# Performance work log

Hardware: AMD Instinct MI355X
Metric: run time of the kernel (lower is better)

## Reference

```python
import jax, jax.numpy as jnp
import numpy as np
import math

N_EMBD = 1024
N_HEAD = 16
B, T = 4, 2048

def setup_inputs() -> dict:
    key = jax.random.key(0)
    k1, k2, k3, k4, k5 = jax.random.split(key, 5)
    C = N_EMBD
    scale_in = 1.0 / math.sqrt(C)
    x = jax.random.normal(k1, (B, T, C), dtype=jnp.float32)
    W_attn = jax.random.normal(k2, (C, 3 * C), dtype=jnp.float32) * scale_in
    b_attn = jax.random.normal(k3, (3 * C,), dtype=jnp.float32) * 0.02
    W_proj = jax.random.normal(k4, (C, C), dtype=jnp.float32) * scale_in
    b_proj = jax.random.normal(k5, (C,), dtype=jnp.float32) * 0.02
    attention_mask = jnp.ones((B, T), dtype=jnp.int32)
    return {"x": x, "W_attn": W_attn, "b_attn": b_attn,
            "W_proj": W_proj, "b_proj": b_proj,
            "attention_mask": attention_mask}

def reference(x, W_attn, b_attn, W_proj, b_proj, attention_mask):
    Bx, Tx, C = x.shape
    H = N_HEAD
    D = C // H
    qkv = x @ W_attn + b_attn                      # [B,T,3C]
    q, k, v = jnp.split(qkv, 3, axis=-1)
    # [B,H,T,D]
    q = q.reshape(Bx, Tx, H, D).transpose(0, 2, 1, 3)
    k = k.reshape(Bx, Tx, H, D).transpose(0, 2, 1, 3)
    v = v.reshape(Bx, Tx, H, D).transpose(0, 2, 1, 3)
    att = jnp.einsum('bhqd,bhkd->bhqk', q, k) * (1.0 / math.sqrt(D))
    causal = jnp.tril(jnp.ones((Tx, Tx), dtype=bool))  # [T,T]
    neg_inf = jnp.float32(-jnp.inf)
    att = jnp.where(causal[None, None, :, :], att, neg_inf)
    pad = (attention_mask != 0)[:, None, None, :]      # [B,1,1,T]
    att = jnp.where(pad, att, neg_inf)
    att = jax.nn.softmax(att, axis=-1)
    y = jnp.einsum('bhqk,bhkd->bhqd', att, v)          # [B,H,T,D]
    y = y.transpose(0, 2, 1, 3).reshape(Bx, Tx, C)
    y = y @ W_proj + b_proj
    return y
```

## Files before the change

### kernel.cpp

```cpp
#include <hip/hip_runtime.h>
#include <hip/hip_bf16.h>
#include <stdint.h>

#define B_ 4
#define T_ 2048
#define C_ 1024
#define H_ 16
#define D_ 64
#define BH_ (B_*H_)
#define M_ (B_*T_)

typedef __attribute__((ext_vector_type(8))) short short8;
typedef __attribute__((ext_vector_type(4))) float f32x4;
typedef __attribute__((ext_vector_type(16))) float f32x16;

#if __has_builtin(__builtin_amdgcn_exp2f)
#define EXP2(x) __builtin_amdgcn_exp2f(x)
#else
#define EXP2(x) exp2f(x)
#endif

#define QSCALE 0.18033688011112043f

__device__ __forceinline__ unsigned short f2bf(float f) {
  union { float f; unsigned int u; } v; v.f = f;
  unsigned int r = v.u + 0x7FFFu + ((v.u >> 16) & 1u);
  return (unsigned short)(r >> 16);
}

__device__ __forceinline__ unsigned int cvtpk_bf16(float lo, float hi) {
  unsigned int r;
  asm("v_cvt_pk_bf16_f32 %0, %1, %2" : "=v"(r) : "v"(lo), "v"(hi));
  return r;
}

__device__ __forceinline__ void gload_lds16(const void* g, void* l) {
  __builtin_amdgcn_global_load_lds(
      (__attribute__((address_space(1))) void*)g,
      (__attribute__((address_space(3))) void*)l, 16, 0, 0);
}

__global__ __launch_bounds__(256) void k_cvt(const float* __restrict__ in,
                                             unsigned short* __restrict__ out, int n) {
  int i = (blockIdx.x * 256 + threadIdx.x) * 4;
  if (i >= n) return;
  float4 v = *reinterpret_cast<const float4*>(in + i);
  union { unsigned short u[4]; unsigned long long ll; } o;
  o.u[0] = f2bf(v.x); o.u[1] = f2bf(v.y); o.u[2] = f2bf(v.z); o.u[3] = f2bf(v.w);
  *reinterpret_cast<unsigned long long*>(out + i) = o.ll;
}

__global__ __launch_bounds__(256) void k_tr(const float* __restrict__ W,
                                            unsigned short* __restrict__ Wt, int K, int N) {
  __shared__ float t[32][33];
  int n0 = blockIdx.x * 32, k0 = blockIdx.y * 32;
  int tx = threadIdx.x, ty = threadIdx.y;
  #pragma unroll
  for (int j = 0; j < 4; j++)
    t[ty + j*8][tx] = W[(size_t)(k0 + ty + j*8) * N + n0 + tx];
  __syncthreads();
  #pragma unroll
  for (int j = 0; j < 4; j++)
    Wt[(size_t)(n0 + ty + j*8) * K + k0 + tx] = f2bf(t[tx][ty + j*8]);
}

template<int QKV>
__global__ __launch_bounds__(512) void k_gemm8(const unsigned short* __restrict__ A,
                                               const unsigned short* __restrict__ Bt,
                                               const float* __restrict__ bias,
                                               void* __restrict__ outp, int N, int K) {
  __shared__ __align__(16) unsigned short Al[2][128*64];
  __shared__ __align__(16) unsigned short Bl[2][256*64];

  const int tid = threadIdx.x;
  const int lane = tid & 63, wv = tid >> 6;
  const int lg = lane >> 4, lr = lane & 15;
  const int wm = wv >> 2, wn = wv & 3;

  const int nwg = gridDim.x * gridDim.y;
  const int l = blockIdx.y * gridDim.x + blockIdx.x;
  const int wg = (l & 7) * (nwg >> 3) + (l >> 3);
  const int m0 = (wg / gridDim.x) * 128;
  const int n0 = (wg % gridDim.x) * 256;

  const int NT = K >> 6;

  auto stageA = [&](int s, int t, int h) {
    int row = tid >> 3, g = tid & 7;
    int gsw = g ^ (row & 7);
    gload_lds16(A + (size_t)(m0 + h*64 + row) * K + t*64 + gsw*8,
                (char*)Al[s] + h*8192 + tid*16);
  };
  auto stageB = [&](int s, int t, int h) {
    #pragma unroll
    for (int u = 0; u < 2; ++u) {
      int gi = tid + u*512;
      int row = gi >> 3, g = gi & 7;
      int gsw = g ^ (row & 7);
      gload_lds16(Bt + (size_t)(n0 + h*128 + row) * K + t*64 + gsw*8,
                  (char*)Bl[s] + h*16384 + gi*16);
    }
  };

  f32x4 acc[2][2][2][2];
  #pragma unroll
  for (int i = 0; i < 2; ++i)
    #pragma unroll
    for (int j = 0; j < 2; ++j)
      #pragma unroll
      for (int p = 0; p < 2; ++p)
        #pragma unroll
        for (int q = 0; q < 2; ++q) acc[i][j][p][q] = (f32x4){0.f,0.f,0.f,0.f};

  stageA(0, 0, 0); stageB(0, 0, 0); stageA(0, 0, 1); stageB(0, 0, 1);
  if (NT > 1) { stageB(1, 1, 0); stageA(1, 1, 0); }
  asm volatile("s_waitcnt vmcnt(3)" ::: "memory");
  __builtin_amdgcn_s_barrier();

#define GPH(MhC, NhC, STAGE, ISPH4, VMOK)  do {                                 \
    short8 af_[2][2], bf_[2][2];                                                \
    _Pragma("unroll") for (int mf = 0; mf < 2; ++mf) {                          \
      int rA = (MhC)*64 + wm*32 + mf*16 + lr;                                   \
      int r7 = rA & 7;                                                          \
      af_[mf][0] = *(const short8*)(Asb + rA*128 + ((lg      ^ r7) << 4));      \
      af_[mf][1] = *(const short8*)(Asb + rA*128 + (((4|lg) ^ r7) << 4));       \
    }                                                                           \
    _Pragma("unroll") for (int nf = 0; nf < 2; ++nf) {                          \
      int rB = (NhC)*128 + wn*32 + nf*16 + lr;                                  \
      int r7 = rB & 7;                                                          \
      bf_[nf][0] = *(const short8*)(Bsb + rB*128 + ((lg      ^ r7) << 4));      \
      bf_[nf][1] = *(const short8*)(Bsb + rB*128 + (((4|lg) ^ r7) << 4));       \
    }                                                                           \
    STAGE;                                                                      \
    __builtin_amdgcn_s_barrier();                                               \
    asm volatile("s_waitcnt lgkmcnt(0)" ::: "memory");                          \
    __builtin_amdgcn_sched_barrier(0);                                          \
    __builtin_amdgcn_s_setprio(1);                                              \
    _Pragma("unroll") for (int mf = 0; mf < 2; ++mf)                            \
      _Pragma("unroll") for (int nf = 0; nf < 2; ++nf) {                        \
        acc[MhC][NhC][mf][nf] = __builtin_amdgcn_mfma_f32_16x16x32_bf16(        \
            af_[mf][0], bf_[nf][0], acc[MhC][NhC][mf][nf], 0, 0, 0);            \
        acc[MhC][NhC][mf][nf] = __builtin_amdgcn_mfma_f32_16x16x32_bf16(        \
            af_[mf][1], bf_[nf][1], acc[MhC][NhC][mf][nf], 0, 0, 0);            \
      }                                                                         \
    __builtin_amdgcn_s_setprio(0);                                              \
    if (ISPH4) {                                                                \
      if (VMOK) asm volatile("s_waitcnt vmcnt(3)" ::: "memory");                \
      else      asm volatile("s_waitcnt vmcnt(0)" ::: "memory");                \
    }                                                                           \
    __builtin_amdgcn_s_barrier();                                               \
  } while (0)

  for (int t = 0; t < NT; ++t) {
    const char* Asb = (const char*)Al[t & 1];
    const char* Bsb = (const char*)Bl[t & 1];
    const int s0 = t & 1, s1 = s0 ^ 1;
    const bool p1 = (t + 1 < NT), p2 = (t + 2 < NT);
    GPH(0, 0, if (p1) stageA(s1, t+1, 1), 0, 0);
    GPH(1, 0, if (p1) stageB(s1, t+1, 1), 0, 0);
    GPH(0, 1, if (p2) stageB(s0, t+2, 0), 0, 0);
    GPH(1, 1, if (p2) stageA(s0, t+2, 0), 1, p2);
  }
#undef GPH

  if (QKV) {
    unsigned short* qb = (unsigned short*)outp;
    const size_t SZ = (size_t)BH_ * T_ * D_;
    #pragma unroll
    for (int Mh = 0; Mh < 2; ++Mh)
      #pragma unroll
      for (int mf = 0; mf < 2; ++mf) {
        int mb = m0 + Mh*64 + wm*32 + mf*16 + lg*4;
        #pragma unroll
        for (int Nh = 0; Nh < 2; ++Nh)
          #pragma unroll
          for (int nf = 0; nf < 2; ++nf) {
            int n = n0 + Nh*128 + wn*32 + nf*16 + lr;
            float bv = bias[n];
            int which = n >> 10, c = n & 1023, h = c >> 6, d = c & 63;
            unsigned short* base = qb + (size_t)which * SZ;
            #pragma unroll
            for (int r = 0; r < 4; ++r) {
              int m = mb + r;
              int bb2 = m >> 11, tt = m & 2047;
              float y = acc[Mh][Nh][mf][nf][r] + bv;
              if (which == 0) y *= QSCALE;
              base[((size_t)(bb2*H_ + h)*T_ + tt)*D_ + d] = f2bf(y);
            }
          }
      }
  } else {
    float* out = (float*)outp;
    #pragma unroll
    for (int Mh = 0; Mh < 2; ++Mh)
      #pragma unroll
      for (int mf = 0; mf < 2; ++mf) {
        int mb = m0 + Mh*64 + wm*32 + mf*16 + lg*4;
        #pragma unroll
        for (int Nh = 0; Nh < 2; ++Nh)
          #pragma unroll
          for (int nf = 0; nf < 2; ++nf) {
            int n = n0 + Nh*128 + wn*32 + nf*16 + lr;
            float bv = bias[n];
            #pragma unroll
            for (int r = 0; r < 4; ++r)
              out[(size_t)(mb + r)*N + n] = acc[Mh][Nh][mf][nf][r] + bv;
          }
      }
  }
}

__global__ __launch_bounds__(256, 2) void k_attn4(const unsigned short* __restrict__ Qb,
                                                  const unsigned short* __restrict__ Kb,
                                                  const unsigned short* __restrict__ Vb,
                                                  const int* __restrict__ amask,
                                                  unsigned short* __restrict__ Yb) {
  __shared__ __align__(16) char pool[32768];

  const int l = blockIdx.y * 16 + blockIdx.x;
  const int local = l >> 3;
  const int tq = 15 - (local >> 3);
  const int bh = (l & 7) * 8 + (local & 7);
  const int bb = bh >> 4, hh = bh & 15;

  const int tid = threadIdx.x;
  const int lane = tid & 63, w = tid >> 6;
  const int hi = lane >> 5, l31 = lane & 31;

  const unsigned short* Qh = Qb + (size_t)bh * (T_*D_);
  const unsigned short* Kh = Kb + (size_t)bh * (T_*D_);
  const unsigned short* Vh = Vb + (size_t)bh * (T_*D_);

  const int kvp = tid & 31, d0v = (tid >> 5) * 8;

  auto stage_load = [&](int i, int b, short8& sv0, short8& sv1, int& nm) {
    const int kv0 = i << 6;
    char* base = pool + b * 16384;
    #pragma unroll
    for (int s = 0; s < 2; ++s) {
      int gi = tid + s * 256;
      int row = gi >> 3, gc = gi & 7;
      gload_lds16(Kh + (size_t)(kv0 + row)*D_ + (gc ^ (row & 7)) * 8, base + gi * 16);
    }
    int kv = kv0 + 2 * kvp;
    sv0 = *reinterpret_cast<const short8*>(Vh + (size_t)kv*D_ + d0v);
    sv1 = *reinterpret_cast<const short8*>(Vh + (size_t)(kv + 1)*D_ + d0v);
    nm = amask[bb*T_ + kv0 + lane];
  };
  auto stage_write = [&](int b, short8 sv0, short8 sv1) {
    unsigned int* vt = (unsigned int*)(pool + b * 16384 + 8192);
    #pragma unroll
    for (int jj = 0; jj < 8; ++jj) {
      int d = d0v + jj;
      unsigned int wd = (unsigned short)sv0[jj] | ((unsigned int)(unsigned short)sv1[jj] << 16);
      vt[d * 32 + (kvp ^ ((d & 7) << 2))] = wd;
    }
  };

  const int nT = 2 * tq + 2;
  const int qbase = tq << 7;
  const int qw = qbase + w * 32;
  const int q  = qw + l31;

  short8 qf[4];
  #pragma unroll
  for (int dt = 0; dt < 4; ++dt)
    qf[dt] = *reinterpret_cast<const short8*>(Qh + (size_t)q*D_ + dt*16 + hi*8);

  f32x16 o0, o1;
  #pragma unroll
  for (int r = 0; r < 16; ++r) { o0[r] = 0.f; o1[r] = 0.f; }
  float mr = -1e30f, ls = 0.f;

  short8 sv0, sv1; int cm;
  stage_load(0, 0, sv0, sv1, cm);
  stage_write(0, sv0, sv1);
  __syncthreads();

  for (int i = 0; i < nT; ++i) {
    const int b = i & 1;
    const bool pf = (i + 1 < nT);
    short8 nv0, nv1; int nm = 0;
    if (pf) stage_load(i + 1, b ^ 1, nv0, nv1, nm);
    const int kv0 = i << 6;

    if (kv0 <= qw + 31) {
      const unsigned short* Klb = (const unsigned short*)(pool + b * 16384);
      const char* Vtb = pool + b * 16384 + 8192;

      f32x16 st0, st1;
      #pragma unroll
      for (int r = 0; r < 16; ++r) { st0[r] = 0.f; st1[r] = 0.f; }
      __builtin_amdgcn_s_setprio(1);
      #pragma unroll
      for (int dt = 0; dt < 4; ++dt) {
        int gg = dt * 2 + hi;
        int ra = l31;
        short8 kf0 = *reinterpret_cast<const short8*>(Klb + ra*64 + (gg ^ (ra & 7)) * 8);
        st0 = __builtin_amdgcn_mfma_f32_32x32x16_bf16(kf0, qf[dt], st0, 0, 0, 0);
        int rb = 32 + l31;
        short8 kf1 = *reinterpret_cast<const short8*>(Klb + rb*64 + (gg ^ (rb & 7)) * 8);
        st1 = __builtin_amdgcn_mfma_f32_32x32x16_bf16(kf1, qf[dt], st1, 0, 0, 0);
      }
      __builtin_amdgcn_s_setprio(0);

      if (kv0 + 63 > qw) {
        #pragma unroll
        for (int r = 0; r < 16; ++r) {
          int kvl = (r & 3) + 8 * (r >> 2) + 4 * hi;
          if (kv0 + kvl      > q) st0[r] = -1e30f;
          if (kv0 + 32 + kvl > q) st1[r] = -1e30f;
        }
      }
      unsigned long long mb = __ballot(cm != 0);
      if (mb != ~0ull) {
        #pragma unroll
        for (int r = 0; r < 16; ++r) {
          int kvl = (r & 3) + 8 * (r >> 2) + 4 * hi;
          if (!((mb >> kvl) & 1))        st0[r] = -1e30f;
          if (!((mb >> (kvl + 32)) & 1)) st1[r] = -1e30f;
        }
      }

      float mm[8];
      #pragma unroll
      for (int r = 0; r < 8; ++r)
        mm[r] = fmaxf(fmaxf(st0[r], st0[r + 8]), fmaxf(st1[r], st1[r + 8]));
      #pragma unroll
      for (int s = 4; s > 0; s >>= 1)
        #pragma unroll
        for (int r = 0; r < s; ++r) mm[r] = fmaxf(mm[r], mm[r + s]);
      float mo = fmaxf(mm[0], __shfl_xor(mm[0], 32));
      if (!__all(mo <= mr + 8.0f)) {
        float mnew = fmaxf(mr, mo);
        float corr = EXP2(mr - mnew);
        ls *= corr;
        #pragma unroll
        for (int r = 0; r < 16; ++r) { o0[r] *= corr; o1[r] *= corr; }
        mr = mnew;
      }
      float rs = 0.f;
      #pragma unroll
      for (int r = 0; r < 16; ++r) {
        st0[r] = EXP2(st0[r] - mr); rs += st0[r];
        st1[r] = EXP2(st1[r] - mr); rs += st1[r];
      }
      rs += __shfl_xor(rs, 32);
      ls += rs;

      unsigned int pw[2][4][2];
      #pragma unroll
      for (int a = 0; a < 4; ++a) {
        pw[0][a][0] = cvtpk_bf16(st0[4*a],   st0[4*a+1]);
        pw[0][a][1] = cvtpk_bf16(st0[4*a+2], st0[4*a+3]);
        pw[1][a][0] = cvtpk_bf16(st1[4*a],   st1[4*a+1]);
        pw[1][a][1] = cvtpk_bf16(st1[4*a+2], st1[4*a+3]);
      }

      #pragma unroll
      for (int kt = 0; kt < 4; ++kt) {
        const int t = kt >> 1, h2 = kt & 1;
        unsigned int send0 = hi ? pw[t][2*h2][0]   : pw[t][2*h2+1][0];
        unsigned int send1 = hi ? pw[t][2*h2][1]   : pw[t][2*h2+1][1];
        unsigned int own0  = hi ? pw[t][2*h2+1][0] : pw[t][2*h2][0];
        unsigned int own1  = hi ? pw[t][2*h2+1][1] : pw[t][2*h2][1];
        unsigned int recv0 = __shfl_xor(send0, 32);
        unsigned int recv1 = __shfl_xor(send1, 32);
        union { unsigned int u[4]; short8 v; } pf2;
        pf2.u[0] = hi ? recv0 : own0;
        pf2.u[1] = hi ? recv1 : own1;
        pf2.u[2] = hi ? own0  : recv0;
        pf2.u[3] = hi ? own1  : recv1;
        int gg = kt * 2 + hi;
        int dA = l31;
        short8 vf0 = *reinterpret_cast<const short8*>(Vtb + dA*128 + ((gg ^ (dA & 7)) * 16));
        int dB = 32 + l31;
        short8 vf1 = *reinterpret_cast<const short8*>(Vtb + dB*128 + ((gg ^ (dB & 7)) * 16));
        __builtin_amdgcn_s_setprio(1);
        o0 = __builtin_amdgcn_mfma_f32_32x32x16_bf16(vf0, pf2.v, o0, 0, 0, 0);
        o1 = __builtin_amdgcn_mfma_f32_32x32x16_bf16(vf1, pf2.v, o1, 0, 0, 0);
        __builtin_amdgcn_s_setprio(0);
      }
    }
    if (pf) { stage_write(b ^ 1, nv0, nv1); cm = nm; }
    __syncthreads();
  }

  float inv = 1.0f / ls;
  size_t rowbase = ((size_t)bb*T_ + q)*C_ + hh*D_;
  #pragma unroll
  for (int a = 0; a < 4; ++a) {
    union { unsigned short h[4]; unsigned long long ll; } y0, y1;
    #pragma unroll
    for (int bq = 0; bq < 4; ++bq) {
      int r = 4*a + bq;
      y0.h[bq] = f2bf(o0[r] * inv);
      y1.h[bq] = f2bf(o1[r] * inv);
    }
    int d0o = 8*a + 4*hi;
    *reinterpret_cast<unsigned long long*>(Yb + rowbase + d0o)      = y0.ll;
    *reinterpret_cast<unsigned long long*>(Yb + rowbase + 32 + d0o) = y1.ll;
  }
}

extern "C" void kernel_launch(void* const* d_in, const int* in_sizes, int n_in,
                              void* d_out, int out_size, void* d_ws, size_t ws_size,
                              hipStream_t stream) {
  const float* x      = (const float*)d_in[0];
  const float* W_attn = (const float*)d_in[1];
  const float* b_attn = (const float*)d_in[2];
  const float* W_proj = (const float*)d_in[3];
  const float* b_proj = (const float*)d_in[4];
  const int*   amask  = (const int*)d_in[5];
  float* out = (float*)d_out;

  char* ws = (char*)d_ws;
  size_t off = 0;
  auto alloc = [&](size_t bytes) { char* p = ws + off; off += (bytes + 255) & ~(size_t)255; return p; };
  unsigned short* xb   = (unsigned short*)alloc((size_t)M_ * C_ * 2);
  unsigned short* Wta  = (unsigned short*)alloc((size_t)3 * C_ * C_ * 2);
  unsigned short* Wtp  = (unsigned short*)alloc((size_t)C_ * C_ * 2);
  unsigned short* qkvb = (unsigned short*)alloc((size_t)3 * BH_ * T_ * D_ * 2);
  unsigned short* Yb   = (unsigned short*)alloc((size_t)M_ * C_ * 2);

  k_cvt<<<(M_ * C_) / 1024, 256, 0, stream>>>(x, xb, M_ * C_);
  k_tr<<<dim3(3*C_/32, C_/32), dim3(32, 8), 0, stream>>>(W_attn, Wta, C_, 3*C_);
  k_tr<<<dim3(C_/32,  C_/32),  dim3(32, 8), 0, stream>>>(W_proj, Wtp, C_, C_);

  k_gemm8<1><<<dim3(3*C_/256, M_/128), 512, 0, stream>>>(xb, Wta, b_attn, qkvb, 3*C_, C_);

  unsigned short* Qb = qkvb;
  unsigned short* Kb = qkvb + (size_t)BH_ * T_ * D_;
  unsigned short* Vb = qkvb + 2 * (size_t)BH_ * T_ * D_;
  k_attn4<<<dim3(16, BH_/1), 256, 0, stream>>>(Qb, Kb, Vb, amask, Yb);

  k_gemm8<0><<<dim3(C_/256, M_/128), 512, 0, stream>>>(Yb, Wtp, b_proj, out, C_, C_);
}
```

Before: 187.5 us.

## Reshape GEMM tile to 256x128 with per-wave 128x32 sub-tiles and B-fragment reuse

Both projection GEMMs now use a 256x128 output tile instead of 128x256. Each wave owns a 128x32 sub-tile, and its B fragments are loaded from LDS once per K-step and reused across two M-halves, which cuts LDS read traffic per MFMA. The pipeline drops from four phases with two-deep prefetch to two phases with one-step-ahead prefetch, and vmcnt waits are adjusted to match. This lowers LDS pressure and barrier count, but leaves less time to hide global-load latency, and the grid shape changes for both GEMMs.

```diff
diff --git a/kernel.cpp b/kernel.cpp
--- a/kernel.cpp
+++ b/kernel.cpp
@@ -69,8 +69,8 @@
                                                const unsigned short* __restrict__ Bt,
                                                const float* __restrict__ bias,
                                                void* __restrict__ outp, int N, int K) {
-  __shared__ __align__(16) unsigned short Al[2][128*64];
-  __shared__ __align__(16) unsigned short Bl[2][256*64];
+  __shared__ __align__(16) unsigned short Al[2][256*64];
+  __shared__ __align__(16) unsigned short Bl[2][128*64];
 
   const int tid = threadIdx.x;
   const int lane = tid & 63, wv = tid >> 6;
@@ -80,86 +80,78 @@
   const int nwg = gridDim.x * gridDim.y;
   const int l = blockIdx.y * gridDim.x + blockIdx.x;
   const int wg = (l & 7) * (nwg >> 3) + (l >> 3);
-  const int m0 = (wg / gridDim.x) * 128;
-  const int n0 = (wg % gridDim.x) * 256;
+  const int m0 = (wg / gridDim.x) * 256;
+  const int n0 = (wg % gridDim.x) * 128;
 
   const int NT = K >> 6;
 
-  auto stageA = [&](int s, int t, int h) {
-    int row = tid >> 3, g = tid & 7;
-    int gsw = g ^ (row & 7);
-    gload_lds16(A + (size_t)(m0 + h*64 + row) * K + t*64 + gsw*8,
-                (char*)Al[s] + h*8192 + tid*16);
+  auto stageA = [&](int s, int t, int u) {
+    int row = u*64 + (tid >> 3), g = tid & 7;
+    gload_lds16(A + (size_t)(m0 + row) * K + t*64 + (g ^ (row & 7)) * 8,
+                (char*)Al + s*32768 + u*8192 + tid*16);
   };
-  auto stageB = [&](int s, int t, int h) {
-    #pragma unroll
-    for (int u = 0; u < 2; ++u) {
-      int gi = tid + u*512;
-      int row = gi >> 3, g = gi & 7;
-      int gsw = g ^ (row & 7);
-      gload_lds16(Bt + (size_t)(n0 + h*128 + row) * K + t*64 + gsw*8,
-                  (char*)Bl[s] + h*16384 + gi*16);
-    }
+  auto stageB = [&](int s, int t, int u) {
+    int row = u*64 + (tid >> 3), g = tid & 7;
+    gload_lds16(Bt + (size_t)(n0 + row) * K + t*64 + (g ^ (row & 7)) * 8,
+                (char*)Bl + s*16384 + u*8192 + tid*16);
   };
 
-  f32x4 acc[2][2][2][2];
-  #pragma unroll
-  for (int i = 0; i < 2; ++i)
-    #pragma unroll
-    for (int j = 0; j < 2; ++j)
-      #pragma unroll
-      for (int p = 0; p < 2; ++p)
-        #pragma unroll
-        for (int q = 0; q < 2; ++q) acc[i][j][p][q] = (f32x4){0.f,0.f,0.f,0.f};
-
-  stageA(0, 0, 0); stageB(0, 0, 0); stageA(0, 0, 1); stageB(0, 0, 1);
-  if (NT > 1) { stageB(1, 1, 0); stageA(1, 1, 0); }
-  asm volatile("s_waitcnt vmcnt(3)" ::: "memory");
+  f32x4 acc[8][2];
+  #pragma unroll
+  for (int i = 0; i < 8; ++i)
+    #pragma unroll
+    for (int j = 0; j < 2; ++j) acc[i][j] = (f32x4){0.f, 0.f, 0.f, 0.f};
+
+  stageB(0,0,0); stageB(0,0,1); stageA(0,0,0); stageA(0,0,2);
+  stageA(0,0,1); stageA(0,0,3);
+  asm volatile("s_waitcnt vmcnt(2)" ::: "memory");
   __builtin_amdgcn_s_barrier();
 
-#define GPH(MhC, NhC, STAGE, ISPH4, VMOK)  do {                                 \
-    short8 af_[2][2], bf_[2][2];                                                \
-    _Pragma("unroll") for (int mf = 0; mf < 2; ++mf) {                          \
-      int rA = (MhC)*64 + wm*32 + mf*16 + lr;                                   \
+#define GPH(MhC, READB, STAGE, WAITE)  do {                                     \
+    short8 af_[4][2];                                                           \
+    _Pragma("unroll") for (int mf = 0; mf < 4; ++mf) {                          \
+      int rA = wm*128 + (MhC)*64 + mf*16 + lr;                                  \
       int r7 = rA & 7;                                                          \
       af_[mf][0] = *(const short8*)(Asb + rA*128 + ((lg      ^ r7) << 4));      \
       af_[mf][1] = *(const short8*)(Asb + rA*128 + (((4|lg) ^ r7) << 4));       \
     }                                                                           \
-    _Pragma("unroll") for (int nf = 0; nf < 2; ++nf) {                          \
-      int rB = (NhC)*128 + wn*32 + nf*16 + lr;                                  \
-      int r7 = rB & 7;                                                          \
-      bf_[nf][0] = *(const short8*)(Bsb + rB*128 + ((lg      ^ r7) << 4));      \
-      bf_[nf][1] = *(const short8*)(Bsb + rB*128 + (((4|lg) ^ r7) << 4));       \
+    if (READB) {                                                                \
+      _Pragma("unroll") for (int nf = 0; nf < 2; ++nf) {                        \
+        int rB = wn*32 + nf*16 + lr;                                            \
+        int r7 = rB & 7;                                                        \
+        bf_[nf][0] = *(const short8*)(Bsb + rB*128 + ((lg      ^ r7) << 4));    \
+        bf_[nf][1] = *(const short8*)(Bsb + rB*128 + (((4|lg) ^ r7) << 4));     \
+      }                                                                         \
     }                                                                           \
     STAGE;                                                                      \
     __builtin_amdgcn_s_barrier();                                               \
     asm volatile("s_waitcnt lgkmcnt(0)" ::: "memory");                          \
     __builtin_amdgcn_sched_barrier(0);                                          \
     __builtin_amdgcn_s_setprio(1);                                              \
-    _Pragma("unroll") for (int mf = 0; mf < 2; ++mf)                            \
-      _Pragma("unroll") for (int nf = 0; nf < 2; ++nf) {                        \
-        acc[MhC][NhC][mf][nf] = __builtin_amdgcn_mfma_f32_16x16x32_bf16(        \
-            af_[mf][0], bf_[nf][0], acc[MhC][NhC][mf][nf], 0, 0, 0);            \
-        acc[MhC][NhC][mf][nf] = __builtin_amdgcn_mfma_f32_16x16x32_bf16(        \
-            af_[mf][1], bf_[nf][1], acc[MhC][NhC][mf][nf], 0, 0, 0);            \
-      }                                                                         \
+    _Pragma("unroll") for (int kh = 0; kh < 2; ++kh)                            \
+      _Pragma("unroll") for (int mf = 0; mf < 4; ++mf)                          \
+        _Pragma("unroll") for (int nf = 0; nf < 2; ++nf)                        \
+          acc[(MhC)*4+mf][nf] = __builtin_amdgcn_mfma_f32_16x16x32_bf16(        \
+              af_[mf][kh], bf_[nf][kh], acc[(MhC)*4+mf][nf], 0, 0, 0);          \
     __builtin_amdgcn_s_setprio(0);                                              \
-    if (ISPH4) {                                                                \
-      if (VMOK) asm volatile("s_waitcnt vmcnt(3)" ::: "memory");                \
-      else      asm volatile("s_waitcnt vmcnt(0)" ::: "memory");                \
-    }                                                                           \
+    WAITE;                                                                      \
     __builtin_amdgcn_s_barrier();                                               \
   } while (0)
 
   for (int t = 0; t < NT; ++t) {
-    const char* Asb = (const char*)Al[t & 1];
-    const char* Bsb = (const char*)Bl[t & 1];
-    const int s0 = t & 1, s1 = s0 ^ 1;
-    const bool p1 = (t + 1 < NT), p2 = (t + 2 < NT);
-    GPH(0, 0, if (p1) stageA(s1, t+1, 1), 0, 0);
-    GPH(1, 0, if (p1) stageB(s1, t+1, 1), 0, 0);
-    GPH(0, 1, if (p2) stageB(s0, t+2, 0), 0, 0);
-    GPH(1, 1, if (p2) stageA(s0, t+2, 0), 1, p2);
+    const char* Asb = (const char*)Al + (t & 1) * 32768;
+    const char* Bsb = (const char*)Bl + (t & 1) * 16384;
+    const int s1 = (t & 1) ^ 1;
+    const bool p1 = (t + 1 < NT);
+    short8 bf_[2][2];
+    GPH(0, 1,
+        if (p1) { stageB(s1,t+1,0); stageB(s1,t+1,1); stageA(s1,t+1,0); stageA(s1,t+1,2); },
+        if (p1) { asm volatile("s_waitcnt vmcnt(4)" ::: "memory"); }
+        else    { asm volatile("s_waitcnt vmcnt(0)" ::: "memory"); });
+    GPH(1, 0,
+        if (p1) { stageA(s1,t+1,1); stageA(s1,t+1,3); },
+        if (p1) { asm volatile("s_waitcnt vmcnt(2)" ::: "memory"); }
+        else    { asm volatile("s_waitcnt vmcnt(0)" ::: "memory"); });
   }
 #undef GPH
 
@@ -167,46 +159,38 @@
     unsigned short* qb = (unsigned short*)outp;
     const size_t SZ = (size_t)BH_ * T_ * D_;
     #pragma unroll
-    for (int Mh = 0; Mh < 2; ++Mh)
-      #pragma unroll
-      for (int mf = 0; mf < 2; ++mf) {
-        int mb = m0 + Mh*64 + wm*32 + mf*16 + lg*4;
-        #pragma unroll
-        for (int Nh = 0; Nh < 2; ++Nh)
-          #pragma unroll
-          for (int nf = 0; nf < 2; ++nf) {
-            int n = n0 + Nh*128 + wn*32 + nf*16 + lr;
-            float bv = bias[n];
-            int which = n >> 10, c = n & 1023, h = c >> 6, d = c & 63;
-            unsigned short* base = qb + (size_t)which * SZ;
-            #pragma unroll
-            for (int r = 0; r < 4; ++r) {
-              int m = mb + r;
-              int bb2 = m >> 11, tt = m & 2047;
-              float y = acc[Mh][Nh][mf][nf][r] + bv;
-              if (which == 0) y *= QSCALE;
-              base[((size_t)(bb2*H_ + h)*T_ + tt)*D_ + d] = f2bf(y);
-            }
-          }
-      }
+    for (int i8 = 0; i8 < 8; ++i8) {
+      int mb = m0 + wm*128 + i8*16 + lg*4;
+      #pragma unroll
+      for (int nf = 0; nf < 2; ++nf) {
+        int n = n0 + wn*32 + nf*16 + lr;
+        float bv = bias[n];
+        int which = n >> 10, c = n & 1023, h = c >> 6, d = c & 63;
+        unsigned short* base = qb + (size_t)which * SZ;
+        #pragma unroll
+        for (int r = 0; r < 4; ++r) {
+          int m = mb + r;
+          int bb2 = m >> 11, tt = m & 2047;
+          float y = acc[i8][nf][r] + bv;
+          if (which == 0) y *= QSCALE;
+          base[((size_t)(bb2*H_ + h)*T_ + tt)*D_ + d] = f2bf(y);
+        }
+      }
+    }
   } else {
     float* out = (float*)outp;
     #pragma unroll
-    for (int Mh = 0; Mh < 2; ++Mh)
-      #pragma unroll
-      for (int mf = 0; mf < 2; ++mf) {
-        int mb = m0 + Mh*64 + wm*32 + mf*16 + lg*4;
-        #pragma unroll
-        for (int Nh = 0; Nh < 2; ++Nh)
-          #pragma unroll
-          for (int nf = 0; nf < 2; ++nf) {
-            int n = n0 + Nh*128 + wn*32 + nf*16 + lr;
-            float bv = bias[n];
-            #pragma unroll
-            for (int r = 0; r < 4; ++r)
-              out[(size_t)(mb + r)*N + n] = acc[Mh][Nh][mf][nf][r] + bv;
-          }
-      }
+    for (int i8 = 0; i8 < 8; ++i8) {
+      int mb = m0 + wm*128 + i8*16 + lg*4;
+      #pragma unroll
+      for (int nf = 0; nf < 2; ++nf) {
+        int n = n0 + wn*32 + nf*16 + lr;
+        float bv = bias[n];
+        #pragma unroll
+        for (int r = 0; r < 4; ++r)
+          out[(size_t)(mb + r)*N + n] = acc[i8][nf][r] + bv;
+      }
+    }
   }
 }
 
@@ -427,12 +411,12 @@
   k_tr<<<dim3(3*C_/32, C_/32), dim3(32, 8), 0, stream>>>(W_attn, Wta, C_, 3*C_);
   k_tr<<<dim3(C_/32,  C_/32),  dim3(32, 8), 0, stream>>>(W_proj, Wtp, C_, C_);
 
-  k_gemm8<1><<<dim3(3*C_/256, M_/128), 512, 0, stream>>>(xb, Wta, b_attn, qkvb, 3*C_, C_);
+  k_gemm8<1><<<dim3(3*C_/128, M_/256), 512, 0, stream>>>(xb, Wta, b_attn, qkvb, 3*C_, C_);
 
   unsigned short* Qb = qkvb;
   unsigned short* Kb = qkvb + (size_t)BH_ * T_ * D_;
   unsigned short* Vb = qkvb + 2 * (size_t)BH_ * T_ * D_;
-  k_attn4<<<dim3(16, BH_/1), 256, 0, stream>>>(Qb, Kb, Vb, amask, Yb);
-
-  k_gemm8<0><<<dim3(C_/256, M_/128), 512, 0, stream>>>(Yb, Wtp, b_proj, out, C_, C_);
-}
+  k_attn4<<<dim3(16, BH_), 256, 0, stream>>>(Qb, Kb, Vb, amask, Yb);
+
+  k_gemm8<0><<<dim3(C_/128, M_/256), 512, 0, stream>>>(Yb, Wtp, b_proj, out, C_, C_);
+}
```

Result: faster. 175.8 us (-6.3%).
